# Optimization experiments

Measured on AMD Instinct MI355X. Metric: run time of the kernel, lower is better.

The kernel has to match this reference:

```python
import jax, jax.numpy as jnp
import numpy as np

FRAME_LEN = 128
FFT_LEN = 128            # smallest power of 2 >= frame_length (TF default)
NUM_SPEC_BINS = FFT_LEN // 2 + 1  # 65
NUM_MEL = 80
SAMPLE_RATE = 16000.0
LOWER_HZ, UPPER_HZ = 80.0, 7600.0


def _hz_to_mel(f):
    # TF's HTK-style mel: 1127 * ln(1 + f/700)
    return 1127.0 * np.log1p(np.asarray(f, dtype=np.float64) / 700.0)


def _linear_to_mel_weight_matrix():
    # Faithful port of tf.signal.linear_to_mel_weight_matrix
    linear_freqs = np.linspace(0.0, SAMPLE_RATE / 2.0, NUM_SPEC_BINS)
    spec_mel = _hz_to_mel(linear_freqs[1:])[:, None]            # [64, 1] (bin 0 zeroed)
    edges = np.linspace(_hz_to_mel(LOWER_HZ), _hz_to_mel(UPPER_HZ), NUM_MEL + 2)
    lower, center, upper = edges[None, :-2], edges[None, 1:-1], edges[None, 2:]
    lower_slopes = (spec_mel - lower) / (center - lower)
    upper_slopes = (upper - spec_mel) / (upper - center)
    w = np.maximum(0.0, np.minimum(lower_slopes, upper_slopes))  # [64, 80]
    return np.pad(w, [[1, 0], [0, 0]]).astype(np.float32)        # [65, 80]


_MEL_W = jnp.asarray(_linear_to_mel_weight_matrix())


def setup_inputs() -> dict:
    key = jax.random.key(0)
    x = jax.random.normal(key, (16, 16384), dtype=jnp.float32)
    return {"x": x}


def reference(x):
    B, N = x.shape
    # pad_end=True with frame_step=1 -> N frames, pad FRAME_LEN-1 zeros at the end
    xp = jnp.pad(x, ((0, 0), (0, FRAME_LEN - 1)))
    idx = jnp.arange(N)[:, None] + jnp.arange(FRAME_LEN)[None, :]  # [N, 128]
    frames = xp[:, idx]                                            # [B, N, 128]
    n = jnp.arange(FRAME_LEN, dtype=jnp.float32)
    window = 0.5 - 0.5 * jnp.cos(2.0 * jnp.pi * n / FRAME_LEN)     # periodic Hann
    stft = jnp.fft.rfft(frames * window, n=FFT_LEN, axis=-1)       # [B, N, 65] complex
    mag = jax.lax.stop_gradient(jnp.abs(stft).astype(jnp.float32))
    mel = mag @ _MEL_W                                             # [B, N, 80]
    return jnp.concatenate([x[..., None], mel], axis=-1)           # [B, N, 81]
```

## Files before the change

### kernel.cpp

```cpp
#include <hip/hip_runtime.h>
#include <hip/hip_fp16.h>
#include <math.h>

#define B_SZ 16
#define N_SZ 16384
#define T_FR 64
#define NTHR 256
#define NBIN 65
#define NMEL 80
#define NCH  81
#define KN   6
#define MSTR 70
#define BSTR 136

typedef _Float16 h8  __attribute__((ext_vector_type(8)));
typedef float    f4  __attribute__((ext_vector_type(4)));
static_assert(sizeof(h8) == 16, "h8 must be 4 VGPRs");


constexpr double cln(double x) {
  int k = 0;
  while (x > 1.5)  { x *= 0.5; ++k; }
  while (x < 0.75) { x *= 2.0; --k; }
  const double y = (x - 1.0) / (x + 1.0);
  const double y2 = y * y;
  double t = y, s = 0.0;
  for (int i = 0; i < 40; ++i) { s += t / (double)(2 * i + 1); t *= y2; }
  return 2.0 * s + (double)k * 0.69314718055994530942;
}
constexpr double melf(double f) { return 1127.0 * cln(1.0 + f / 700.0); }

struct MelTab {
  int   kbe[NMEL];
  float w[NMEL][KN];
  constexpr MelTab() : kbe{}, w{} {
    const double mlo = melf(80.0), mhi = melf(7600.0);
    const double dm  = (mhi - mlo) / 81.0;
    for (int j = 0; j < NMEL; ++j) {
      const double lower = mlo + dm * (double)j;
      const double upper = lower + 2.0 * dm;
      int kb = 64;
      for (int k = 1; k < NBIN; ++k) {
        const double m = melf(125.0 * (double)k);
        const double a = m - lower, b2 = upper - m;
        if ((a < b2 ? a : b2) > 0.0) { kb = k; break; }
      }
      if (kb > NBIN - KN) kb = NBIN - KN;
      kbe[j] = kb;
      for (int r = 0; r < KN; ++r) {
        const int k = kb + r;
        double ww = 0.0;
        if (k >= 1 && k < NBIN) {
          const double m = melf(125.0 * (double)k);
          const double a = (m - lower) / dm, b2 = (upper - m) / dm;
          ww = a < b2 ? a : b2;
          if (ww < 0.0) ww = 0.0;
        }
        w[j][r] = (float)ww;
      }
    }
  }
};
constexpr MelTab MT{};

template <int J0>
__device__ __forceinline__ void mel20(const __half* mrow, float* srow) {
#pragma unroll
  for (int jj = 0; jj < 20; ++jj) {
    const int j = J0 + jj;
    float acc = 0.0f;
#pragma unroll
    for (int r = 0; r < KN; ++r) {
      if (MT.w[j][r] != 0.0f)
        acc = fmaf(MT.w[j][r], __half2float(mrow[MT.kbe[j] + r]), acc);
    }
    srow[1 + j] = acc;
  }
}

__global__ __launch_bounds__(NTHR, 3) void melspec_kernel(const float* __restrict__ x,
                                                          float* __restrict__ out) {
  __shared__ __align__(16) unsigned char smem[160 * BSTR * 2];
  __shared__ float  xs[192];
  __shared__ __half magh[T_FR * MSTR];

  const int tid = threadIdx.x;
  const int t0  = blockIdx.x * T_FR;
  const int b   = blockIdx.y;

  const float* xrow = x + (size_t)b * N_SZ;
  if (tid < 192) xs[tid] = (t0 + tid < N_SZ) ? xrow[t0 + tid] : 0.0f;

  {
    _Float16* bt = (_Float16*)smem;
    const float w0 = 6.2831853071795864769f / 128.0f;
    for (int e = tid; e < NBIN * 128; e += NTHR) {
      const int k = e >> 7, n = e & 127;
      const float wh = 0.5f - 0.5f * __cosf(w0 * (float)n);
      float sv, cv;
      __sincosf(w0 * (float)((k * n) & 127), &sv, &cv);
      bt[k * BSTR + n]        = (_Float16)(wh * cv);
      bt[(80 + k) * BSTR + n] = (_Float16)(-wh * sv);
    }
    for (int e = tid; e < 15 * 128; e += NTHR) {
      const int c = e >> 7, n = e & 127;
      bt[(65 + c) * BSTR + n]  = (_Float16)0.f;
      bt[(145 + c) * BSTR + n] = (_Float16)0.f;
    }
  }
  __syncthreads();

  const int wv = tid >> 6;
  const int ln = tid & 63;
  const int lr = ln & 15;
  const int lg = ln >> 4;

  f4 acc[10];
  {
    const f4 z = {0.f, 0.f, 0.f, 0.f};
#pragma unroll
    for (int i = 0; i < 10; ++i) acc[i] = z;
  }

  const _Float16* btp = (const _Float16*)smem;
#pragma unroll
  for (int kk = 0; kk < 4; ++kk) {
    h8 a;
    const float* ap = xs + 16 * wv + lr + kk * 32 + lg * 8;
#pragma unroll
    for (int j = 0; j < 8; ++j) a[j] = (_Float16)ap[j];
    h8 bfr[10];
#pragma unroll
    for (int nt = 0; nt < 10; ++nt)
      bfr[nt] = *(const h8*)(btp + (nt * 16 + lr) * BSTR + kk * 32 + lg * 8);
#pragma unroll
    for (int nt = 0; nt < 10; ++nt)
      acc[nt] = __builtin_amdgcn_mfma_f32_16x16x32_f16(a, bfr[nt], acc[nt], 0, 0, 0);
  }

#pragma unroll
  for (int r = 0; r < 5; ++r) {
    if (r < 4 || lr == 0) {
      const int k = r * 16 + lr;
#pragma unroll
      for (int v = 0; v < 4; ++v) {
        const int t = 16 * wv + lg * 4 + v;
        const float re = acc[r][v], im = acc[r + 5][v];
        magh[t * MSTR + k] = __float2half(sqrtf(re * re + im * im));
      }
    }
  }
  __syncthreads();

  float* stage = (float*)smem;
  {
    const int t = tid & 63, q = tid >> 6;
    const __half* mrow = magh + t * MSTR;
    float* srow = stage + t * NCH;
    if (q == 0) srow[0] = xs[t];
    switch (q) {
      case 0:  mel20<0>(mrow, srow);  break;
      case 1:  mel20<20>(mrow, srow); break;
      case 2:  mel20<40>(mrow, srow); break;
      default: mel20<60>(mrow, srow); break;
    }
  }
  __syncthreads();

  float* orow = out + ((size_t)b * N_SZ + t0) * NCH;
#pragma unroll
  for (int i = 0; i < 5; ++i) {
    const int f = i * 1024 + tid * 4;
    *(float4*)(orow + f) = *(const float4*)(stage + f);
  }
  if (tid < 64) orow[5120 + tid] = stage[5120 + tid];
}

extern "C" void kernel_launch(void* const* d_in, const int* in_sizes, int n_in,
                              void* d_out, int out_size, void* d_ws, size_t ws_size,
                              hipStream_t stream) {
  const float* x = (const float*)d_in[0];
  float* out = (float*)d_out;
  dim3 grid(N_SZ / T_FR, B_SZ);
  dim3 block(NTHR);
  hipLaunchKernelGGL(melspec_kernel, grid, block, 0, stream, x, out);
}
```

Measured before the change: 120.0 us.

## Precompute DFT and mel tables globally; use MFMA for mel projection

```diff
diff --git a/kernel.cpp b/kernel.cpp
--- a/kernel.cpp
+++ b/kernel.cpp
@@ -6,164 +6,136 @@
 #define N_SZ 16384
 #define T_FR 64
 #define NTHR 256
-#define NBIN 65
 #define NMEL 80
 #define NCH  81
-#define KN   6
-#define MSTR 70
-#define BSTR 136
 
 typedef _Float16 h8  __attribute__((ext_vector_type(8)));
+typedef _Float16 h4  __attribute__((ext_vector_type(4)));
 typedef float    f4  __attribute__((ext_vector_type(4)));
 static_assert(sizeof(h8) == 16, "h8 must be 4 VGPRs");
 
+__device__ _Float16 g_tab[2688 * 8];
 
-constexpr double cln(double x) {
-  int k = 0;
-  while (x > 1.5)  { x *= 0.5; ++k; }
-  while (x < 0.75) { x *= 2.0; --k; }
-  const double y = (x - 1.0) / (x + 1.0);
-  const double y2 = y * y;
-  double t = y, s = 0.0;
-  for (int i = 0; i < 40; ++i) { s += t / (double)(2 * i + 1); t *= y2; }
-  return 2.0 * s + (double)k * 0.69314718055994530942;
-}
-constexpr double melf(double f) { return 1127.0 * cln(1.0 + f / 700.0); }
-
-struct MelTab {
-  int   kbe[NMEL];
-  float w[NMEL][KN];
-  constexpr MelTab() : kbe{}, w{} {
-    const double mlo = melf(80.0), mhi = melf(7600.0);
-    const double dm  = (mhi - mlo) / 81.0;
-    for (int j = 0; j < NMEL; ++j) {
-      const double lower = mlo + dm * (double)j;
-      const double upper = lower + 2.0 * dm;
-      int kb = 64;
-      for (int k = 1; k < NBIN; ++k) {
-        const double m = melf(125.0 * (double)k);
-        const double a = m - lower, b2 = upper - m;
-        if ((a < b2 ? a : b2) > 0.0) { kb = k; break; }
-      }
-      if (kb > NBIN - KN) kb = NBIN - KN;
-      kbe[j] = kb;
-      for (int r = 0; r < KN; ++r) {
-        const int k = kb + r;
-        double ww = 0.0;
-        if (k >= 1 && k < NBIN) {
-          const double m = melf(125.0 * (double)k);
-          const double a = (m - lower) / dm, b2 = (upper - m) / dm;
-          ww = a < b2 ? a : b2;
-          if (ww < 0.0) ww = 0.0;
-        }
-        w[j][r] = (float)ww;
-      }
+__global__ void build_tables() {
+  const int u = blockIdx.x * blockDim.x + threadIdx.x;
+  if (u >= 2688) return;
+  const float w0 = 6.2831853071795864769f / 128.0f;
+  h8 res;
+  if (u < 2048) {
+    const int ln = u & 63, kk = (u >> 6) & 3, pol = (u >> 8) & 1, g = u >> 9;
+    const int bin = 16 * g + (ln & 15);
+    const int k0  = kk * 32 + ((ln >> 4) & 3) * 8;
+#pragma unroll
+    for (int j = 0; j < 8; ++j) {
+      const int k = k0 + j;
+      const float wh = 0.5f - 0.5f * __cosf(w0 * (float)k);
+      float sv, cv;
+      __sincosf(w0 * (float)((bin * k) & 127), &sv, &cv);
+      res[j] = (_Float16)(pol ? (-wh * sv) : (wh * cv));
+    }
+  } else {
+    const int u2 = u - 2048;
+    const int ln = u2 & 63, kkB = (u2 >> 6) & 1, jt = u2 >> 7;
+    const int mj = 16 * jt + (ln & 15);
+    const int b0 = kkB * 32 + ((ln >> 4) & 3) * 8;
+    const float mlo = 1127.0f * logf(1.0f + 80.0f / 700.0f);
+    const float mhi = 1127.0f * logf(1.0f + 7600.0f / 700.0f);
+    const float dm  = (mhi - mlo) / 81.0f;
+#pragma unroll
+    for (int j = 0; j < 8; ++j) {
+      const int bin = b0 + j;
+      const float m  = 1127.0f * logf(1.0f + 125.0f * (float)bin / 700.0f);
+      const float lower = mlo + dm * (float)mj;
+      const float ls = (m - lower) / dm;
+      const float us = (lower + 2.0f * dm - m) / dm;
+      res[j] = (_Float16)fmaxf(0.0f, fminf(ls, us));
     }
   }
-};
-constexpr MelTab MT{};
-
-template <int J0>
-__device__ __forceinline__ void mel20(const __half* mrow, float* srow) {
-#pragma unroll
-  for (int jj = 0; jj < 20; ++jj) {
-    const int j = J0 + jj;
-    float acc = 0.0f;
-#pragma unroll
-    for (int r = 0; r < KN; ++r) {
-      if (MT.w[j][r] != 0.0f)
-        acc = fmaf(MT.w[j][r], __half2float(mrow[MT.kbe[j] + r]), acc);
-    }
-    srow[1 + j] = acc;
-  }
+  ((h8*)g_tab)[u] = res;
 }
 
-__global__ __launch_bounds__(NTHR, 3) void melspec_kernel(const float* __restrict__ x,
-                                                          float* __restrict__ out) {
-  __shared__ __align__(16) unsigned char smem[160 * BSTR * 2];
-  __shared__ float  xs[192];
-  __shared__ __half magh[T_FR * MSTR];
+__global__ __launch_bounds__(NTHR) void melspec_kernel(const float* __restrict__ x,
+                                                       float* __restrict__ out) {
+  __shared__ __align__(16) _Float16 xh2[184 * 8];
+  __shared__ __align__(16) _Float16 magT[512 * 8];
+  __shared__ float xs[64];
+  __shared__ __align__(16) float stage[T_FR * NCH];
 
   const int tid = threadIdx.x;
   const int t0  = blockIdx.x * T_FR;
   const int b   = blockIdx.y;
-
   const float* xrow = x + (size_t)b * N_SZ;
-  if (tid < 192) xs[tid] = (t0 + tid < N_SZ) ? xrow[t0 + tid] : 0.0f;
-
-  {
-    _Float16* bt = (_Float16*)smem;
-    const float w0 = 6.2831853071795864769f / 128.0f;
-    for (int e = tid; e < NBIN * 128; e += NTHR) {
-      const int k = e >> 7, n = e & 127;
-      const float wh = 0.5f - 0.5f * __cosf(w0 * (float)n);
-      float sv, cv;
-      __sincosf(w0 * (float)((k * n) & 127), &sv, &cv);
-      bt[k * BSTR + n]        = (_Float16)(wh * cv);
-      bt[(80 + k) * BSTR + n] = (_Float16)(-wh * sv);
-    }
-    for (int e = tid; e < 15 * 128; e += NTHR) {
-      const int c = e >> 7, n = e & 127;
-      bt[(65 + c) * BSTR + n]  = (_Float16)0.f;
-      bt[(145 + c) * BSTR + n] = (_Float16)0.f;
-    }
-  }
-  __syncthreads();
 
   const int wv = tid >> 6;
   const int ln = tid & 63;
   const int lr = ln & 15;
-  const int lg = ln >> 4;
+  const int lg = (ln >> 4) & 3;
 
-  f4 acc[10];
+  if (tid < 64) xs[tid] = xrow[t0 + tid];
+  if (tid < 184) {
+    h8 tmp;
+#pragma unroll
+    for (int j = 0; j < 8; ++j) {
+      const int gix = t0 + tid + j;
+      tmp[j] = (_Float16)((gix < N_SZ) ? xrow[gix] : 0.0f);
+    }
+    *(h8*)(xh2 + tid * 8) = tmp;
+  }
+  const h8* tabv = (const h8*)g_tab;
+  h8 aRe[4], aIm[4];
+#pragma unroll
+  for (int kk = 0; kk < 4; ++kk) {
+    aRe[kk] = tabv[((wv * 2 + 0) * 4 + kk) * 64 + ln];
+    aIm[kk] = tabv[((wv * 2 + 1) * 4 + kk) * 64 + ln];
+  }
+  __syncthreads();
+
+#pragma unroll
+  for (int ft = 0; ft < 4; ++ft) {
+    f4 cr = {0.f, 0.f, 0.f, 0.f};
+    f4 ci = {0.f, 0.f, 0.f, 0.f};
+#pragma unroll
+    for (int kk = 0; kk < 4; ++kk) {
+      const h8 bb = *(const h8*)(xh2 + (16 * ft + 32 * kk + 8 * lg + lr) * 8);
+      cr = __builtin_amdgcn_mfma_f32_16x16x32_f16(aRe[kk], bb, cr, 0, 0, 0);
+      ci = __builtin_amdgcn_mfma_f32_16x16x32_f16(aIm[kk], bb, ci, 0, 0, 0);
+    }
+    h4 pk;
+#pragma unroll
+    for (int v = 0; v < 4; ++v) {
+      const float re = cr[v], im = ci[v];
+      pk[v] = (_Float16)sqrtf(re * re + im * im);
+    }
+    const int bg = 2 * wv + (lg >> 1);
+    *(h4*)(magT + ((bg * 64 + 16 * ft + lr) * 8 + 4 * (lg & 1))) = pk;
+  }
+  h8 aW[10];
+#pragma unroll
+  for (int q = 0; q < 10; ++q) aW[q] = tabv[2048 + q * 64 + ln];
+  __syncthreads();
+
+  f4 acc[5];
   {
     const f4 z = {0.f, 0.f, 0.f, 0.f};
 #pragma unroll
-    for (int i = 0; i < 10; ++i) acc[i] = z;
+    for (int i = 0; i < 5; ++i) acc[i] = z;
   }
-
-  const _Float16* btp = (const _Float16*)smem;
 #pragma unroll
-  for (int kk = 0; kk < 4; ++kk) {
-    h8 a;
-    const float* ap = xs + 16 * wv + lr + kk * 32 + lg * 8;
+  for (int kkB = 0; kkB < 2; ++kkB) {
+    const h8 bb = *(const h8*)(magT + ((kkB * 4 + lg) * 64 + 16 * wv + lr) * 8);
 #pragma unroll
-    for (int j = 0; j < 8; ++j) a[j] = (_Float16)ap[j];
-    h8 bfr[10];
+    for (int jt = 0; jt < 5; ++jt)
+      acc[jt] = __builtin_amdgcn_mfma_f32_16x16x32_f16(aW[jt * 2 + kkB], bb, acc[jt], 0, 0, 0);
+  }
+  {
+    const int fr = 16 * wv + lr;
+    float* srow = stage + fr * NCH;
+    if (lg == 0) srow[0] = xs[fr];
 #pragma unroll
-    for (int nt = 0; nt < 10; ++nt)
-      bfr[nt] = *(const h8*)(btp + (nt * 16 + lr) * BSTR + kk * 32 + lg * 8);
+    for (int jt = 0; jt < 5; ++jt)
 #pragma unroll
-    for (int nt = 0; nt < 10; ++nt)
-      acc[nt] = __builtin_amdgcn_mfma_f32_16x16x32_f16(a, bfr[nt], acc[nt], 0, 0, 0);
-  }
-
-#pragma unroll
-  for (int r = 0; r < 5; ++r) {
-    if (r < 4 || lr == 0) {
-      const int k = r * 16 + lr;
-#pragma unroll
-      for (int v = 0; v < 4; ++v) {
-        const int t = 16 * wv + lg * 4 + v;
-        const float re = acc[r][v], im = acc[r + 5][v];
-        magh[t * MSTR + k] = __float2half(sqrtf(re * re + im * im));
-      }
-    }
-  }
-  __syncthreads();
-
-  float* stage = (float*)smem;
-  {
-    const int t = tid & 63, q = tid >> 6;
-    const __half* mrow = magh + t * MSTR;
-    float* srow = stage + t * NCH;
-    if (q == 0) srow[0] = xs[t];
-    switch (q) {
-      case 0:  mel20<0>(mrow, srow);  break;
-      case 1:  mel20<20>(mrow, srow); break;
-      case 2:  mel20<40>(mrow, srow); break;
-      default: mel20<60>(mrow, srow); break;
-    }
+      for (int v = 0; v < 4; ++v)
+        srow[1 + 16 * jt + 4 * lg + v] = acc[jt][v];
   }
   __syncthreads();
 
@@ -181,6 +153,7 @@
                               hipStream_t stream) {
   const float* x = (const float*)d_in[0];
   float* out = (float*)d_out;
+  hipLaunchKernelGGL(build_tables, dim3(11), dim3(256), 0, stream);
   dim3 grid(N_SZ / T_FR, B_SZ);
   dim3 block(NTHR);
   hipLaunchKernelGGL(melspec_kernel, grid, block, 0, stream, x, out);
```

Result: faster. 106.3 us (-11.4%).
